# Kernel tuning notes

Hardware: AMD Instinct MI355X
Metric: run time of the kernel (lower is better)

The kernel has to match this reference:

```python
import jax, jax.numpy as jnp
import numpy as np

N = 4096
E = 131072
IN_CH, E_CH, HID, OUT = 512, 64, 256, 16
K, J = 2, 3
REWEIGHT = ((E_CH + HID) / (IN_CH + HID)) ** 0.5


def gcn(x, W, b, src, dst, dinv):
    # x: [B, N, F] -> [B, N, H]; symmetric-normalized aggregation with self-loops (PyG GCNConv)
    h = x @ W
    norm = dinv[src] * dinv[dst]                      # [E]
    msg = jnp.take(h, src, axis=-2) * norm[:, None]   # [B, E, H]
    agg = jnp.zeros_like(h).at[:, dst, :].add(msg)
    out = agg + h * (dinv * dinv)[:, None]            # self-loop term, norm_ii = deg_i^-1
    return out + b


def setup_inputs() -> dict:
    key = jax.random.key(0)
    ks = jax.random.split(key, 12)
    x = jax.random.normal(ks[0], (1, N, IN_CH), jnp.float32)
    edge_index = jax.random.randint(ks[1], (2, E), 0, N)
    e_noise = jax.random.normal(ks[2], (K + J, N, E_CH), jnp.float32)
    eps = jax.random.normal(ks[3], (J, N, OUT), jnp.float32)
    def glorot(k, fan_in, fan_out):
        s = (6.0 / (fan_in + fan_out)) ** 0.5
        return jax.random.uniform(k, (fan_in, fan_out), jnp.float32, -s, s)
    W1 = glorot(ks[4], IN_CH, HID); b1 = jnp.zeros((HID,), jnp.float32)
    We = glorot(ks[5], E_CH, HID); be = jnp.zeros((HID,), jnp.float32)
    Wmu = glorot(ks[6], HID, OUT); bmu = jnp.zeros((OUT,), jnp.float32)
    Wsig = glorot(ks[7], HID, OUT); bsig = jnp.zeros((OUT,), jnp.float32)
    rk_lgt = jax.random.uniform(ks[8], (1, OUT), jnp.float32, -6.0, 0.0)
    return {"x": x, "edge_index": edge_index, "e_noise": e_noise, "eps": eps,
            "W1": W1, "b1": b1, "We": We, "be": be,
            "Wmu": Wmu, "bmu": bmu, "Wsig": Wsig, "bsig": bsig, "rk_lgt": rk_lgt}


def reference(x, edge_index, e_noise, eps, W1, b1, We, be, Wmu, bmu, Wsig, bsig, rk_lgt):
    src, dst = edge_index[0], edge_index[1]
    deg = jnp.zeros((N,), jnp.float32).at[dst].add(1.0) + 1.0  # self-loops
    dinv = jax.lax.rsqrt(deg)

    hidden_x = jax.nn.relu(gcn(x, W1, b1, src, dst, dinv))          # [1, N, HID]
    e = e_noise * REWEIGHT                                          # [K+J, N, E_CH]
    hidden_e = gcn(e, We, be, src, dst, dinv)                       # [K+J, N, HID]
    hidden1 = hidden_x + hidden_e                                   # [K+J, N, HID]

    p_signal = jnp.mean(hidden_x ** 2)
    p_noise = jnp.mean(hidden_e ** 2, axis=(-2, -1))                # [K+J]
    snr = p_signal / p_noise

    mu = gcn(hidden1, Wmu, bmu, src, dst, dinv)                     # [K+J, N, OUT]
    sigma = gcn(hidden1, Wsig, bsig, src, dst, dinv)                # [K+J, N, OUT]

    emb_mu = mu[K:]
    emb_logvar = sigma[K:]
    std = jnp.exp(emb_logvar * 0.5)
    z = eps * std + emb_mu                                          # [J, N, OUT]

    # GraphDecoder, gdc='ip', dropout=0 (eval): z_scaled = z, adj = sigmoid(z z^T)
    rk = jnp.sqrt(jax.nn.sigmoid(rk_lgt))                           # [1, OUT]
    adj_lgt = jnp.einsum('bnd,bmd->bnm', z, z)                      # [J, N, N]
    adj_ = jax.nn.sigmoid(adj_lgt)
    z_scaled = z
    return (adj_, mu, sigma, z, z_scaled, eps, rk, snr)
```

## Files before the change

kernel.cpp:

```cpp
#include <hip/hip_runtime.h>

#define NN     4096
#define NE     131072
#define IN_CH  512
#define E_CH   64
#define HID    256
#define OUT_CH 16
#define KK     2
#define JJ     3
#define NB     5
#define REWEIGHT 0.6454972243679028f

#define O_ADJ  0L
#define O_MU   50331648L
#define O_SG   50659328L
#define O_Z    50987008L
#define O_ZS   51183616L
#define O_EPS  51380224L
#define O_RK   51576832L
#define O_SNR  51576848L

__device__ __forceinline__ float fast_sigmoid(float x) {
    float e = __expf(-x);
    return __builtin_amdgcn_rcpf(1.f + e);
}


__global__ void k_deg(const int* __restrict__ dst, int* __restrict__ degi) {
    int i = blockIdx.x * 256 + threadIdx.x;
    if (i < NE) atomicAdd(&degi[dst[i]], 1);
}

__global__ void __launch_bounds__(1024) k_scan(const int* __restrict__ degi,
                       int* __restrict__ rowptr, int* __restrict__ cursor,
                       float* __restrict__ dinv) {
    __shared__ int sums[1024];
    int t = threadIdx.x;
    int d0[4], v[4];
    int s = 0;
#pragma unroll
    for (int i = 0; i < 4; ++i) { d0[i] = degi[t * 4 + i]; v[i] = s; s += d0[i]; }
    sums[t] = s;
    __syncthreads();
    for (int off = 1; off < 1024; off <<= 1) {
        int a = (t >= off) ? sums[t - off] : 0;
        __syncthreads();
        sums[t] += a;
        __syncthreads();
    }
    int base = (t > 0) ? sums[t - 1] : 0;
#pragma unroll
    for (int i = 0; i < 4; ++i) {
        rowptr[t * 4 + i] = base + v[i];
        cursor[t * 4 + i] = base + v[i];
        dinv[t * 4 + i] = rsqrtf((float)d0[i] + 1.0f);
    }
    if (t == 1023) rowptr[4096] = sums[1023];
}

__global__ void k_fill(const int* __restrict__ src, const int* __restrict__ dst,
                       const float* __restrict__ dinv,
                       int* __restrict__ cursor, int* __restrict__ esrc,
                       float* __restrict__ enorm) {
    int i = blockIdx.x * 256 + threadIdx.x;
    if (i >= NE) return;
    int s = src[i], d = dst[i];
    int pos = atomicAdd(&cursor[d], 1);
    esrc[pos] = s;
    enorm[pos] = dinv[s] * dinv[d];
}


__global__ void __launch_bounds__(256) k_gemm_x(const float* __restrict__ x,
                         const float* __restrict__ W1, float* __restrict__ h) {
    __shared__ float xs[8][IN_CH];
    long r0 = (long)blockIdx.x * 8;
    int c = threadIdx.x;
    for (int idx = c; idx < 8 * IN_CH; idx += 256) {
        int rr = idx >> 9, k = idx & 511;
        xs[rr][k] = x[(r0 + rr) * IN_CH + k];
    }
    __syncthreads();
    float acc[8] = {};
#pragma unroll 4
    for (int k = 0; k < IN_CH; ++k) {
        float w = W1[k * HID + c];
#pragma unroll
        for (int rr = 0; rr < 8; ++rr) acc[rr] = fmaf(xs[rr][k], w, acc[rr]);
    }
#pragma unroll
    for (int rr = 0; rr < 8; ++rr) h[(r0 + rr) * HID + c] = acc[rr];
}

__global__ void __launch_bounds__(256) k_agg_x(const float* __restrict__ h,
                        const int* __restrict__ rowptr,
                        const int* __restrict__ esrc, const float* __restrict__ enorm,
                        const float* __restrict__ dinv, const float* __restrict__ b1,
                        float* __restrict__ hx, float* __restrict__ psum) {
    int n = blockIdx.x;
    int c = threadIdx.x;
    int beg = rowptr[n], end = rowptr[n + 1];
    float dv = dinv[n];
    float acc = h[(long)n * HID + c] * dv * dv + b1[c];
    for (int j = beg; j < end; ++j)
        acc = fmaf(h[(long)esrc[j] * HID + c], enorm[j], acc);
    acc = fmaxf(acc, 0.f);
    hx[(long)n * HID + c] = acc;
    float sq = acc * acc;
#pragma unroll
    for (int off = 32; off; off >>= 1) sq += __shfl_down(sq, off, 64);
    __shared__ float red[4];
    if ((threadIdx.x & 63) == 0) red[threadIdx.x >> 6] = sq;
    __syncthreads();
    if (threadIdx.x == 0) atomicAdd(&psum[0], red[0] + red[1] + red[2] + red[3]);
}

__global__ void __launch_bounds__(256) k_agg_e(const float* __restrict__ e,
                        const int* __restrict__ rowptr, const int* __restrict__ esrc,
                        const float* __restrict__ enorm, const float* __restrict__ dinv,
                        float* __restrict__ u) {
    int n = blockIdx.x * 4 + (threadIdx.x >> 6);
    int c = threadIdx.x & 63;
    int beg = rowptr[n], end = rowptr[n + 1];
    float dv = dinv[n];
    float d2 = dv * dv;
    float acc[NB];
#pragma unroll
    for (int b = 0; b < NB; ++b) acc[b] = e[((long)b * NN + n) * E_CH + c] * d2;
    for (int j = beg; j < end; ++j) {
        int s = esrc[j];
        float w = enorm[j];
        long base = (long)s * E_CH + c;
#pragma unroll
        for (int b = 0; b < NB; ++b)
            acc[b] = fmaf(e[(long)b * NN * E_CH + base], w, acc[b]);
    }
#pragma unroll
    for (int b = 0; b < NB; ++b) u[((long)b * NN + n) * E_CH + c] = acc[b] * REWEIGHT;
}

__global__ void __launch_bounds__(256) k_gemm_e(const float* __restrict__ u,
                         const float* __restrict__ We,
                         const float* __restrict__ be, float* __restrict__ he,
                         float* __restrict__ psum) {
    __shared__ float us[8][E_CH];
    long r0 = (long)blockIdx.x * 8;
    int c = threadIdx.x;
    for (int idx = c; idx < 8 * E_CH; idx += 256) {
        int rr = idx >> 6, k = idx & 63;
        us[rr][k] = u[(r0 + rr) * E_CH + k];
    }
    __syncthreads();
    float acc[8] = {};
#pragma unroll
    for (int k = 0; k < E_CH; ++k) {
        float w = We[k * HID + c];
#pragma unroll
        for (int rr = 0; rr < 8; ++rr) acc[rr] = fmaf(us[rr][k], w, acc[rr]);
    }
    float bias = be[c];
    float sq = 0.f;
#pragma unroll
    for (int rr = 0; rr < 8; ++rr) {
        float v = acc[rr] + bias;
        he[(r0 + rr) * HID + c] = v;
        sq += v * v;
    }
#pragma unroll
    for (int off = 32; off; off >>= 1) sq += __shfl_down(sq, off, 64);
    __shared__ float red[4];
    if ((threadIdx.x & 63) == 0) red[threadIdx.x >> 6] = sq;
    __syncthreads();
    if (threadIdx.x == 0) {
        int b = blockIdx.x >> 9;
        atomicAdd(&psum[1 + b], red[0] + red[1] + red[2] + red[3]);
    }
}

__global__ void __launch_bounds__(256) k_gemm_ms(const float* __restrict__ hx,
                          const float* __restrict__ he,
                          const float* __restrict__ Wmu, const float* __restrict__ Wsg,
                          float* __restrict__ hmu, float* __restrict__ hsg) {
    int o = threadIdx.x & 15;
    int nn = threadIdx.x >> 4;
    int n = blockIdx.x * 16 + nn;
    int b = blockIdx.y;
    const float* px = &hx[(long)n * HID];
    const float* pe = &he[((long)b * NN + n) * HID];
    float amu = 0.f, asg = 0.f;
#pragma unroll 4
    for (int k = 0; k < HID; ++k) {
        float h1 = px[k] + pe[k];
        amu = fmaf(h1, Wmu[k * OUT_CH + o], amu);
        asg = fmaf(h1, Wsg[k * OUT_CH + o], asg);
    }
    long idx = ((long)b * NN + n) * OUT_CH + o;
    hmu[idx] = amu;
    hsg[idx] = asg;
}

__global__ void __launch_bounds__(256) k_agg16(const int* __restrict__ rowptr,
                        const int* __restrict__ esrc,
                        const float* __restrict__ enorm, const float* __restrict__ dinv,
                        const float* __restrict__ hmu, const float* __restrict__ hsg,
                        const float* __restrict__ bmu, const float* __restrict__ bsg,
                        float* __restrict__ omu, float* __restrict__ osg) {
    int p = blockIdx.x * 4 + (threadIdx.x >> 6);
    int lane = threadIdx.x & 63;
    int n = p & (NN - 1);
    int b = p >> 12;
    int es = lane >> 4, c = lane & 15;
    int beg = rowptr[n], end = rowptr[n + 1];
    const float* pm = &hmu[(long)b * NN * OUT_CH];
    const float* ps = &hsg[(long)b * NN * OUT_CH];
    float am = 0.f, as = 0.f;
    for (int j = beg + es; j < end; j += 4) {
        int s = esrc[j];
        float w = enorm[j];
        am = fmaf(pm[(long)s * OUT_CH + c], w, am);
        as = fmaf(ps[(long)s * OUT_CH + c], w, as);
    }
    am += __shfl_xor(am, 16, 64); as += __shfl_xor(as, 16, 64);
    am += __shfl_xor(am, 32, 64); as += __shfl_xor(as, 32, 64);
    float dv = dinv[n];
    float d2 = dv * dv;
    long base = ((long)b * NN + n) * OUT_CH;
    if (lane < 16) {
        omu[base + c] = am + pm[(long)n * OUT_CH + c] * d2 + bmu[c];
    } else if (lane < 32) {
        osg[base + c] = as + ps[(long)n * OUT_CH + c] * d2 + bsg[c];
    }
}


__global__ void k_z(const float* __restrict__ omu, const float* __restrict__ osg,
                    const float* __restrict__ eps,
                    float* __restrict__ oz, float* __restrict__ ozs, float* __restrict__ oeps,
                    const float* __restrict__ rk_lgt, const float* __restrict__ psum,
                    float* __restrict__ ork, float* __restrict__ osnr) {
    long i = (long)blockIdx.x * 256 + threadIdx.x;
    float mu = omu[(long)KK * NN * OUT_CH + i];
    float lv = osg[(long)KK * NN * OUT_CH + i];
    float ep = eps[i];
    float z = fmaf(ep, expf(0.5f * lv), mu);
    oz[i] = z;
    ozs[i] = z;
    oeps[i] = ep;
    if (blockIdx.x == 0) {
        int t = threadIdx.x;
        if (t < 16) ork[t] = sqrtf(1.f / (1.f + expf(-rk_lgt[t])));
        if (t >= 16 && t < 16 + NB) osnr[t - 16] = psum[0] / psum[1 + (t - 16)];
    }
}

__global__ void __launch_bounds__(256) k_adj(const float* __restrict__ z,
                                             float* __restrict__ adj) {
    __shared__ float zaT[16][132];
    __shared__ float zbT[16][132];
    int b  = blockIdx.z;
    int bi = blockIdx.y;
    int bj = blockIdx.x;
    const float* zbase = &z[(long)b * NN * OUT_CH];
    int tid = threadIdx.x;
    for (int l = tid; l < 128 * 16; l += 256) {
        int r = l >> 4, c = l & 15;
        zaT[c][r] = zbase[((long)bi * 128 + r) * OUT_CH + c];
        zbT[c][r] = zbase[((long)bj * 128 + r) * OUT_CH + c];
    }
    __syncthreads();
    int tr = tid >> 4, tc = tid & 15;
    float acc[8][8] = {};
#pragma unroll
    for (int d = 0; d < OUT_CH; ++d) {
        float4 a0 = *reinterpret_cast<const float4*>(&zaT[d][tr * 8]);
        float4 a1 = *reinterpret_cast<const float4*>(&zaT[d][tr * 8 + 4]);
        float4 b0 = *reinterpret_cast<const float4*>(&zbT[d][tc * 8]);
        float4 b1 = *reinterpret_cast<const float4*>(&zbT[d][tc * 8 + 4]);
        float av[8] = {a0.x, a0.y, a0.z, a0.w, a1.x, a1.y, a1.z, a1.w};
        float bv[8] = {b0.x, b0.y, b0.z, b0.w, b1.x, b1.y, b1.z, b1.w};
#pragma unroll
        for (int i = 0; i < 8; ++i)
#pragma unroll
            for (int j = 0; j < 8; ++j) acc[i][j] = fmaf(av[i], bv[j], acc[i][j]);
    }
#pragma unroll
    for (int i = 0; i < 8; ++i) {
        long row = (long)bi * 128 + tr * 8 + i;
        float* orow = &adj[((long)b * NN + row) * NN + (long)bj * 128 + tc * 8];
        float4 o0, o1;
        o0.x = fast_sigmoid(acc[i][0]); o0.y = fast_sigmoid(acc[i][1]);
        o0.z = fast_sigmoid(acc[i][2]); o0.w = fast_sigmoid(acc[i][3]);
        o1.x = fast_sigmoid(acc[i][4]); o1.y = fast_sigmoid(acc[i][5]);
        o1.z = fast_sigmoid(acc[i][6]); o1.w = fast_sigmoid(acc[i][7]);
        *reinterpret_cast<float4*>(&orow[0]) = o0;
        *reinterpret_cast<float4*>(&orow[4]) = o1;
    }
}


extern "C" void kernel_launch(void* const* d_in, const int* in_sizes, int n_in,
                              void* d_out, int out_size, void* d_ws, size_t ws_size,
                              hipStream_t stream) {
    const float* x      = (const float*)d_in[0];
    const int*   eidx   = (const int*)d_in[1];
    const float* enoise = (const float*)d_in[2];
    const float* eps    = (const float*)d_in[3];
    const float* W1     = (const float*)d_in[4];
    const float* b1     = (const float*)d_in[5];
    const float* We     = (const float*)d_in[6];
    const float* be     = (const float*)d_in[7];
    const float* Wmu    = (const float*)d_in[8];
    const float* bmu    = (const float*)d_in[9];
    const float* Wsg    = (const float*)d_in[10];
    const float* bsg    = (const float*)d_in[11];
    const float* rk_lgt = (const float*)d_in[12];

    const int* src = eidx;
    const int* dst = eidx + NE;

    float* out = (float*)d_out;
    char*  ws  = (char*)d_ws;

    int*   degi   = (int*)ws;
    int*   rowptr = degi + 4096;
    int*   cursor = rowptr + 4097 + 3;
    int*   esrc   = cursor + 4096;
    float* enorm  = (float*)(esrc + NE);
    float* dinv   = enorm + NE;
    float* psum   = dinv + 4096;
    float* h_x    = psum + 16;
    float* hx     = h_x + (long)NN * HID;
    float* u_e    = hx + (long)NN * HID;
    float* he     = u_e + (long)NB * NN * E_CH;
    float* h_mu   = he + (long)NB * NN * HID;
    float* h_sg   = h_mu + (long)NB * NN * OUT_CH;

    float* omu = out + O_MU;
    float* osg = out + O_SG;

    hipMemsetAsync(degi, 0, NN * sizeof(int), stream);
    hipMemsetAsync(psum, 0, 16 * sizeof(float), stream);

    k_deg<<<NE / 256, 256, 0, stream>>>(dst, degi);
    k_scan<<<1, 1024, 0, stream>>>(degi, rowptr, cursor, dinv);
    k_fill<<<NE / 256, 256, 0, stream>>>(src, dst, dinv, cursor, esrc, enorm);

    k_gemm_x<<<NN / 8, 256, 0, stream>>>(x, W1, h_x);
    k_agg_x<<<NN, 256, 0, stream>>>(h_x, rowptr, esrc, enorm, dinv, b1, hx, psum);

    k_agg_e<<<NN / 4, 256, 0, stream>>>(enoise, rowptr, esrc, enorm, dinv, u_e);
    k_gemm_e<<<NB * NN / 8, 256, 0, stream>>>(u_e, We, be, he, psum);

    k_gemm_ms<<<dim3(NN / 16, NB), 256, 0, stream>>>(hx, he, Wmu, Wsg, h_mu, h_sg);
    k_agg16<<<NB * NN / 4, 256, 0, stream>>>(rowptr, esrc, enorm, dinv,
                                             h_mu, h_sg, bmu, bsg, omu, osg);

    k_z<<<(long)JJ * NN * OUT_CH / 256, 256, 0, stream>>>(omu, osg, eps,
                                                          out + O_Z, out + O_ZS, out + O_EPS,
                                                          rk_lgt, psum, out + O_RK, out + O_SNR);

    k_adj<<<dim3(NN / 128, NN / 128, JJ), 256, 0, stream>>>(out + O_Z, out);
}
```

Measured before the change: 543.3 us.

## Eliminate hidden_e materialization via Gram-matrix SNR and folded We weights

Removes the NB×N×HID hidden_e GEMM and buffer. The noise power is computed algebraically from the 64-wide aggregated noise using the Gram matrix We·Weᵀ, the vector We·be and be·be. The mu/sigma projections use the precomputed products We·Wmu and We·Wsg plus folded biases. Degree counting, the x GEMM and the weight precompute are merged into one multi-role launch, the two aggregations into another, and the z computation is fused into the final aggregation, which reduces launches and memory traffic. Changing the summation order shifts floating-point rounding. The adjacency kernel, which likely dominates runtime, is left untouched.

```diff
diff --git a/kernel.cpp b/kernel.cpp
--- a/kernel.cpp
+++ b/kernel.cpp
@@ -25,11 +25,81 @@
     return __builtin_amdgcn_rcpf(1.f + e);
 }
 
-
-__global__ void k_deg(const int* __restrict__ dst, int* __restrict__ degi) {
-    int i = blockIdx.x * 256 + threadIdx.x;
-    if (i < NE) atomicAdd(&degi[dst[i]], 1);
-}
+__global__ void __launch_bounds__(256) k_mega1(
+        const int* __restrict__ dst, int* __restrict__ degi,
+        const float* __restrict__ x, const float* __restrict__ W1, float* __restrict__ h,
+        const float* __restrict__ We, const float* __restrict__ Wmu,
+        const float* __restrict__ Wsg, const float* __restrict__ be,
+        float* __restrict__ G, float* __restrict__ Wem, float* __restrict__ Wes,
+        float* __restrict__ bem, float* __restrict__ bes,
+        float* __restrict__ vG, float* __restrict__ cbe) {
+    int bid = blockIdx.x;
+    int t = threadIdx.x;
+    if (bid < 512) {
+        int i = bid * 256 + t;
+        atomicAdd(&degi[dst[i]], 1);
+        return;
+    }
+    if (bid < 1024) {
+        __shared__ float xs[8][IN_CH];
+        long r0 = (long)(bid - 512) * 8;
+        for (int idx = t; idx < 8 * IN_CH; idx += 256) {
+            int rr = idx >> 9, k = idx & 511;
+            xs[rr][k] = x[(r0 + rr) * IN_CH + k];
+        }
+        __syncthreads();
+        float acc[8] = {};
+#pragma unroll 4
+        for (int k = 0; k < IN_CH; ++k) {
+            float w = W1[k * HID + t];
+#pragma unroll
+            for (int rr = 0; rr < 8; ++rr) acc[rr] = fmaf(xs[rr][k], w, acc[rr]);
+        }
+#pragma unroll
+        for (int rr = 0; rr < 8; ++rr) h[(r0 + rr) * HID + t] = acc[rr];
+        return;
+    }
+    int wb = bid - 1024;
+    if (wb < 16) {
+        int r = wb * 4 + (t >> 6), c = t & 63;
+        const float* wr = &We[(long)r * HID];
+        const float* wc = &We[(long)c * HID];
+        float s = 0.f;
+#pragma unroll 4
+        for (int o = 0; o < HID; ++o) s = fmaf(wr[o], wc[o], s);
+        G[r * 64 + c] = s;
+    } else if (wb < 18) {
+        const float* Wx = (wb == 16) ? Wmu : Wsg;
+        float* Wo = (wb == 16) ? Wem : Wes;
+        float* bo = (wb == 16) ? bem : bes;
+        int j = t & 15, c0 = t >> 4;
+#pragma unroll
+        for (int cc = 0; cc < 4; ++cc) {
+            int c = c0 + cc * 16;
+            const float* wc = &We[(long)c * HID];
+            float s = 0.f;
+            for (int o = 0; o < HID; ++o) s = fmaf(wc[o], Wx[o * OUT_CH + j], s);
+            Wo[c * OUT_CH + j] = s;
+        }
+        if (t < 16) {
+            float s = 0.f;
+            for (int o = 0; o < HID; ++o) s = fmaf(be[o], Wx[o * OUT_CH + t], s);
+            bo[t] = s;
+        }
+    } else {
+        if (t < 64) {
+            const float* wc = &We[(long)t * HID];
+            float s = 0.f;
+            for (int o = 0; o < HID; ++o) s = fmaf(wc[o], be[o], s);
+            vG[t] = s;
+        } else if (t == 64) {
+            float s = 0.f;
+            for (int o = 0; o < HID; ++o) s = fmaf(be[o], be[o], s);
+            cbe[0] = s;
+        }
+    }
+}
+
 
 __global__ void __launch_bounds__(1024) k_scan(const int* __restrict__ degi,
                        int* __restrict__ rowptr, int* __restrict__ cursor,
@@ -70,141 +140,118 @@
     enorm[pos] = dinv[s] * dinv[d];
 }
 
-
-__global__ void __launch_bounds__(256) k_gemm_x(const float* __restrict__ x,
-                         const float* __restrict__ W1, float* __restrict__ h) {
-    __shared__ float xs[8][IN_CH];
-    long r0 = (long)blockIdx.x * 8;
-    int c = threadIdx.x;
-    for (int idx = c; idx < 8 * IN_CH; idx += 256) {
-        int rr = idx >> 9, k = idx & 511;
-        xs[rr][k] = x[(r0 + rr) * IN_CH + k];
-    }
-    __syncthreads();
-    float acc[8] = {};
-#pragma unroll 4
-    for (int k = 0; k < IN_CH; ++k) {
-        float w = W1[k * HID + c];
-#pragma unroll
-        for (int rr = 0; rr < 8; ++rr) acc[rr] = fmaf(xs[rr][k], w, acc[rr]);
-    }
-#pragma unroll
-    for (int rr = 0; rr < 8; ++rr) h[(r0 + rr) * HID + c] = acc[rr];
-}
-
-__global__ void __launch_bounds__(256) k_agg_x(const float* __restrict__ h,
-                        const int* __restrict__ rowptr,
-                        const int* __restrict__ esrc, const float* __restrict__ enorm,
-                        const float* __restrict__ dinv, const float* __restrict__ b1,
-                        float* __restrict__ hx, float* __restrict__ psum) {
-    int n = blockIdx.x;
-    int c = threadIdx.x;
-    int beg = rowptr[n], end = rowptr[n + 1];
-    float dv = dinv[n];
-    float acc = h[(long)n * HID + c] * dv * dv + b1[c];
-    for (int j = beg; j < end; ++j)
-        acc = fmaf(h[(long)esrc[j] * HID + c], enorm[j], acc);
-    acc = fmaxf(acc, 0.f);
-    hx[(long)n * HID + c] = acc;
-    float sq = acc * acc;
-#pragma unroll
-    for (int off = 32; off; off >>= 1) sq += __shfl_down(sq, off, 64);
-    __shared__ float red[4];
-    if ((threadIdx.x & 63) == 0) red[threadIdx.x >> 6] = sq;
-    __syncthreads();
-    if (threadIdx.x == 0) atomicAdd(&psum[0], red[0] + red[1] + red[2] + red[3]);
-}
-
-__global__ void __launch_bounds__(256) k_agg_e(const float* __restrict__ e,
-                        const int* __restrict__ rowptr, const int* __restrict__ esrc,
-                        const float* __restrict__ enorm, const float* __restrict__ dinv,
-                        float* __restrict__ u) {
-    int n = blockIdx.x * 4 + (threadIdx.x >> 6);
-    int c = threadIdx.x & 63;
+__global__ void __launch_bounds__(256) k_mega2(
+        const float* __restrict__ h, const int* __restrict__ rowptr,
+        const int* __restrict__ esrc, const float* __restrict__ enorm,
+        const float* __restrict__ dinv, const float* __restrict__ b1,
+        float* __restrict__ hx, float* __restrict__ psum,
+        const float* __restrict__ e, float* __restrict__ u,
+        const float* __restrict__ G, const float* __restrict__ vG,
+        const float* __restrict__ cbe) {
+    __shared__ float gs[64][65];
+    __shared__ float us[4][NB][64];
+    __shared__ float red4[4];
+    int bid = blockIdx.x;
+    int t = threadIdx.x;
+    if (bid < 4096) {
+        int n = bid;
+        int beg = rowptr[n], end = rowptr[n + 1];
+        float dv = dinv[n];
+        float acc = h[(long)n * HID + t] * dv * dv + b1[t];
+        for (int j = beg; j < end; ++j)
+            acc = fmaf(h[(long)esrc[j] * HID + t], enorm[j], acc);
+        acc = fmaxf(acc, 0.f);
+        hx[(long)n * HID + t] = acc;
+        float sq = acc * acc;
+#pragma unroll
+        for (int off = 32; off; off >>= 1) sq += __shfl_down(sq, off, 64);
+        if ((t & 63) == 0) red4[t >> 6] = sq;
+        __syncthreads();
+        if (t == 0) atomicAdd(&psum[0], red4[0] + red4[1] + red4[2] + red4[3]);
+        return;
+    }
+    for (int l = t; l < 64 * 64; l += 256) gs[l >> 6][l & 63] = G[l];
+    int w = t >> 6;
+    int n = (bid - 4096) * 4 + w;
+    int c = t & 63;
     int beg = rowptr[n], end = rowptr[n + 1];
     float dv = dinv[n];
     float d2 = dv * dv;
-    float acc[NB];
-#pragma unroll
-    for (int b = 0; b < NB; ++b) acc[b] = e[((long)b * NN + n) * E_CH + c] * d2;
+    float ub[NB];
+#pragma unroll
+    for (int b = 0; b < NB; ++b) ub[b] = e[((long)b * NN + n) * E_CH + c] * d2;
     for (int j = beg; j < end; ++j) {
         int s = esrc[j];
-        float w = enorm[j];
+        float wn = enorm[j];
         long base = (long)s * E_CH + c;
 #pragma unroll
         for (int b = 0; b < NB; ++b)
-            acc[b] = fmaf(e[(long)b * NN * E_CH + base], w, acc[b]);
-    }
-#pragma unroll
-    for (int b = 0; b < NB; ++b) u[((long)b * NN + n) * E_CH + c] = acc[b] * REWEIGHT;
-}
-
-__global__ void __launch_bounds__(256) k_gemm_e(const float* __restrict__ u,
-                         const float* __restrict__ We,
-                         const float* __restrict__ be, float* __restrict__ he,
-                         float* __restrict__ psum) {
-    __shared__ float us[8][E_CH];
-    long r0 = (long)blockIdx.x * 8;
-    int c = threadIdx.x;
-    for (int idx = c; idx < 8 * E_CH; idx += 256) {
-        int rr = idx >> 6, k = idx & 63;
-        us[rr][k] = u[(r0 + rr) * E_CH + k];
+            ub[b] = fmaf(e[(long)b * NN * E_CH + base], wn, ub[b]);
+    }
+#pragma unroll
+    for (int b = 0; b < NB; ++b) {
+        ub[b] *= REWEIGHT;
+        u[((long)b * NN + n) * E_CH + c] = ub[b];
+        us[w][b][c] = ub[b];
     }
     __syncthreads();
-    float acc[8] = {};
-#pragma unroll
-    for (int k = 0; k < E_CH; ++k) {
-        float w = We[k * HID + c];
-#pragma unroll
-        for (int rr = 0; rr < 8; ++rr) acc[rr] = fmaf(us[rr][k], w, acc[rr]);
-    }
-    float bias = be[c];
-    float sq = 0.f;
-#pragma unroll
-    for (int rr = 0; rr < 8; ++rr) {
-        float v = acc[rr] + bias;
-        he[(r0 + rr) * HID + c] = v;
-        sq += v * v;
-    }
-#pragma unroll
-    for (int off = 32; off; off >>= 1) sq += __shfl_down(sq, off, 64);
-    __shared__ float red[4];
-    if ((threadIdx.x & 63) == 0) red[threadIdx.x >> 6] = sq;
-    __syncthreads();
-    if (threadIdx.x == 0) {
-        int b = blockIdx.x >> 9;
-        atomicAdd(&psum[1 + b], red[0] + red[1] + red[2] + red[3]);
+    float t5[NB] = {};
+    for (int c2 = 0; c2 < 64; ++c2) {
+        float g = gs[c][c2];
+#pragma unroll
+        for (int b = 0; b < NB; ++b) t5[b] = fmaf(g, us[w][b][c2], t5[b]);
+    }
+    float vr = vG[c];
+    float cb = cbe[0];
+#pragma unroll
+    for (int b = 0; b < NB; ++b) {
+        float r = ub[b] * (t5[b] + 2.f * vr);
+#pragma unroll
+        for (int off = 32; off; off >>= 1) r += __shfl_xor(r, off, 64);
+        if (c == 0) atomicAdd(&psum[1 + b], r + cb);
     }
 }
 
 __global__ void __launch_bounds__(256) k_gemm_ms(const float* __restrict__ hx,
-                          const float* __restrict__ he,
+                          const float* __restrict__ u,
                           const float* __restrict__ Wmu, const float* __restrict__ Wsg,
+                          const float* __restrict__ Wem, const float* __restrict__ Wes,
+                          const float* __restrict__ bem, const float* __restrict__ bes,
                           float* __restrict__ hmu, float* __restrict__ hsg) {
     int o = threadIdx.x & 15;
     int nn = threadIdx.x >> 4;
     int n = blockIdx.x * 16 + nn;
     int b = blockIdx.y;
     const float* px = &hx[(long)n * HID];
-    const float* pe = &he[((long)b * NN + n) * HID];
-    float amu = 0.f, asg = 0.f;
+    const float* pu = &u[((long)b * NN + n) * E_CH];
+    float amu = bem[o], asg = bes[o];
 #pragma unroll 4
     for (int k = 0; k < HID; ++k) {
-        float h1 = px[k] + pe[k];
+        float h1 = px[k];
         amu = fmaf(h1, Wmu[k * OUT_CH + o], amu);
         asg = fmaf(h1, Wsg[k * OUT_CH + o], asg);
+    }
+#pragma unroll 4
+    for (int k = 0; k < E_CH; ++k) {
+        float uv = pu[k];
+        amu = fmaf(uv, Wem[k * OUT_CH + o], amu);
+        asg = fmaf(uv, Wes[k * OUT_CH + o], asg);
     }
     long idx = ((long)b * NN + n) * OUT_CH + o;
     hmu[idx] = amu;
     hsg[idx] = asg;
 }
 
-__global__ void __launch_bounds__(256) k_agg16(const int* __restrict__ rowptr,
-                        const int* __restrict__ esrc,
-                        const float* __restrict__ enorm, const float* __restrict__ dinv,
-                        const float* __restrict__ hmu, const float* __restrict__ hsg,
-                        const float* __restrict__ bmu, const float* __restrict__ bsg,
-                        float* __restrict__ omu, float* __restrict__ osg) {
+__global__ void __launch_bounds__(256) k_agg16z(const int* __restrict__ rowptr,
+        const int* __restrict__ esrc, const float* __restrict__ enorm,
+        const float* __restrict__ dinv,
+        const float* __restrict__ hmu, const float* __restrict__ hsg,
+        const float* __restrict__ bmu, const float* __restrict__ bsg,
+        const float* __restrict__ eps,
+        float* __restrict__ omu, float* __restrict__ osg,
+        float* __restrict__ oz, float* __restrict__ ozs, float* __restrict__ oeps,
+        const float* __restrict__ rk_lgt, const float* __restrict__ psum,
+        float* __restrict__ ork, float* __restrict__ osnr) {
     int p = blockIdx.x * 4 + (threadIdx.x >> 6);
     int lane = threadIdx.x & 63;
     int n = p & (NN - 1);
@@ -224,32 +271,24 @@
     am += __shfl_xor(am, 32, 64); as += __shfl_xor(as, 32, 64);
     float dv = dinv[n];
     float d2 = dv * dv;
+    float vmu = am + pm[(long)n * OUT_CH + c] * d2 + bmu[c];
+    float vsg = as + ps[(long)n * OUT_CH + c] * d2 + bsg[c];
     long base = ((long)b * NN + n) * OUT_CH;
     if (lane < 16) {
-        omu[base + c] = am + pm[(long)n * OUT_CH + c] * d2 + bmu[c];
+        omu[base + c] = vmu;
     } else if (lane < 32) {
-        osg[base + c] = as + ps[(long)n * OUT_CH + c] * d2 + bsg[c];
-    }
-}
-
-
-__global__ void k_z(const float* __restrict__ omu, const float* __restrict__ osg,
-                    const float* __restrict__ eps,
-                    float* __restrict__ oz, float* __restrict__ ozs, float* __restrict__ oeps,
-                    const float* __restrict__ rk_lgt, const float* __restrict__ psum,
-                    float* __restrict__ ork, float* __restrict__ osnr) {
-    long i = (long)blockIdx.x * 256 + threadIdx.x;
-    float mu = omu[(long)KK * NN * OUT_CH + i];
-    float lv = osg[(long)KK * NN * OUT_CH + i];
-    float ep = eps[i];
-    float z = fmaf(ep, expf(0.5f * lv), mu);
-    oz[i] = z;
-    ozs[i] = z;
-    oeps[i] = ep;
-    if (blockIdx.x == 0) {
-        int t = threadIdx.x;
-        if (t < 16) ork[t] = sqrtf(1.f / (1.f + expf(-rk_lgt[t])));
-        if (t >= 16 && t < 16 + NB) osnr[t - 16] = psum[0] / psum[1 + (t - 16)];
+        osg[base + c] = vsg;
+    }
+    if (b >= KK && lane < 16) {
+        long zi = ((long)(b - KK) * NN + n) * OUT_CH + c;
+        float ep = eps[zi];
+        float zv = fmaf(ep, expf(0.5f * vsg), vmu);
+        oz[zi] = zv; ozs[zi] = zv; oeps[zi] = ep;
+    }
+    if (blockIdx.x == 0 && threadIdx.x < 16 + NB) {
+        int tt = threadIdx.x;
+        if (tt < 16) ork[tt] = sqrtf(1.f / (1.f + expf(-rk_lgt[tt])));
+        else osnr[tt - 16] = psum[0] / psum[1 + (tt - 16)];
     }
 }
 
@@ -319,45 +358,52 @@
     const int* dst = eidx + NE;
 
     float* out = (float*)d_out;
-    char*  ws  = (char*)d_ws;
-
-    int*   degi   = (int*)ws;
-    int*   rowptr = degi + 4096;
+    char*  wsb = (char*)d_ws;
+
+    int*   degi   = (int*)wsb;
+    float* psum   = (float*)(degi + 4096);
+    int*   rowptr = (int*)(psum + 16);
     int*   cursor = rowptr + 4097 + 3;
     int*   esrc   = cursor + 4096;
     float* enorm  = (float*)(esrc + NE);
     float* dinv   = enorm + NE;
-    float* psum   = dinv + 4096;
-    float* h_x    = psum + 16;
+    float* h_x    = dinv + 4096;
     float* hx     = h_x + (long)NN * HID;
-    float* u_e    = hx + (long)NN * HID;
-    float* he     = u_e + (long)NB * NN * E_CH;
-    float* h_mu   = he + (long)NB * NN * HID;
-    float* h_sg   = h_mu + (long)NB * NN * OUT_CH;
+    float* u      = hx + (long)NN * HID;
+    float* hmu    = u + (long)NB * NN * E_CH;
+    float* hsg    = hmu + (long)NB * NN * OUT_CH;
+    float* G      = hsg + (long)NB * NN * OUT_CH;
+    float* Wem    = G + 64 * 64;
+    float* Wes    = Wem + 64 * OUT_CH;
+    float* bem    = Wes + 64 * OUT_CH;
+    float* bes    = bem + OUT_CH;
+    float* vG     = bes + OUT_CH;
+    float* cbe    = vG + 64;
 
     float* omu = out + O_MU;
     float* osg = out + O_SG;
 
-    hipMemsetAsync(degi, 0, NN * sizeof(int), stream);
-    hipMemsetAsync(psum, 0, 16 * sizeof(float), stream);
-
-    k_deg<<<NE / 256, 256, 0, stream>>>(dst, degi);
+    hipMemsetAsync(degi, 0, 4112 * sizeof(int), stream);
+
+    k_mega1<<<1043, 256, 0, stream>>>(dst, degi, x, W1, h_x,
+                                      We, Wmu, Wsg, be,
+                                      G, Wem, Wes, bem, bes, vG, cbe);
+
     k_scan<<<1, 1024, 0, stream>>>(degi, rowptr, cursor, dinv);
+
     k_fill<<<NE / 256, 256, 0, stream>>>(src, dst, dinv, cursor, esrc, enorm);
 
-    k_gemm_x<<<NN / 8, 256, 0, stream>>>(x, W1, h_x);
-    k_agg_x<<<NN, 256, 0, stream>>>(h_x, rowptr, esrc, enorm, dinv, b1, hx, psum);
-
-    k_agg_e<<<NN / 4, 256, 0, stream>>>(enoise, rowptr, esrc, enorm, dinv, u_e);
-    k_gemm_e<<<NB * NN / 8, 256, 0, stream>>>(u_e, We, be, he, psum);
-
-    k_gemm_ms<<<dim3(NN / 16, NB), 256, 0, stream>>>(hx, he, Wmu, Wsg, h_mu, h_sg);
-    k_agg16<<<NB * NN / 4, 256, 0, stream>>>(rowptr, esrc, enorm, dinv,
-                                             h_mu, h_sg, bmu, bsg, omu, osg);
-
-    k_z<<<(long)JJ * NN * OUT_CH / 256, 256, 0, stream>>>(omu, osg, eps,
-                                                          out + O_Z, out + O_ZS, out + O_EPS,
-                                                          rk_lgt, psum, out + O_RK, out + O_SNR);
+    k_mega2<<<4096 + NN / 4, 256, 0, stream>>>(h_x, rowptr, esrc, enorm, dinv, b1,
+                                               hx, psum, enoise, u, G, vG, cbe);
+
+    k_gemm_ms<<<dim3(NN / 16, NB), 256, 0, stream>>>(hx, u, Wmu, Wsg, Wem, Wes,
+                                                     bem, bes, hmu, hsg);
+
+    k_agg16z<<<NB * NN / 4, 256, 0, stream>>>(rowptr, esrc, enorm, dinv,
+                                              hmu, hsg, bmu, bsg, eps,
+                                              omu, osg,
+                                              out + O_Z, out + O_ZS, out + O_EPS,
+                                              rk_lgt, psum, out + O_RK, out + O_SNR);
 
     k_adj<<<dim3(NN / 128, NN / 128, JJ), 256, 0, stream>>>(out + O_Z, out);
 }
```

Result: slower. 787.3 us (+44.9%).
